# Kernel tuning notes

Measured on AMD Instinct MI355X. Metric: run time of the kernel, lower is better.

Reference implementation:

```python
import jax, jax.numpy as jnp
import numpy as np

GRID_RES = 128
K_PATHS = 8
SIGMA = 0.8
OFFSETS = jnp.array([[0,0,0],[0,0,1],[0,1,0],[0,1,1],[1,0,0],[1,0,1],[1,1,0],[1,1,1]], dtype=jnp.int32)


def setup_inputs() -> dict:
    key = jax.random.key(0)
    ks = jax.random.split(key, 8)
    N = 500000
    M = 500000
    x_source_ref = jax.random.uniform(ks[0], (N, 3), jnp.float32)
    x_source_curr = jnp.clip(x_source_ref + 0.02 * jax.random.normal(ks[1], (N, 3), jnp.float32), 0.0, 1.0)
    x_query_ref = jax.random.uniform(ks[2], (M, 3), jnp.float32)
    def dense(k, fan_in, fan_out):
        return (jax.random.normal(k, (fan_in, fan_out), jnp.float32) / np.sqrt(fan_in)).astype(jnp.float32)
    return {
        'x_query_ref': x_query_ref,
        'x_source_ref': x_source_ref,
        'x_source_curr': x_source_curr,
        'W_f': dense(ks[3], 3, 3), 'b_f': jnp.zeros((3,), jnp.float32),
        'W_d1': dense(ks[4], 24, 64), 'b_d1': jnp.zeros((64,), jnp.float32),
        'W_d2': dense(ks[5], 64, 64), 'b_d2': jnp.zeros((64,), jnp.float32),
        'W_d3': dense(ks[6], 64, 3), 'b_d3': jnp.zeros((3,), jnp.float32),
    }


def _p2g(content, coords):
    # 8-corner trilinear scatter-add: content [N,C] at float coords [N,3] -> flat grid [R^3, C]
    R = GRID_RES
    base = jnp.floor(coords).astype(jnp.int32)            # [N,3]
    d = coords - base.astype(coords.dtype)                # [N,3] fractional part
    off = OFFSETS[:, None, :]                             # [8,1,3]
    w = jnp.prod(jnp.where(off == 1, d[None], 1.0 - d[None]), axis=-1)  # [8,N]
    idx = base[None] + off                                # [8,N,3]
    flat = (idx[..., 0] * R + idx[..., 1]) * R + idx[..., 2]            # [8,N]
    C = content.shape[-1]
    vals = content[None] * w[..., None]                   # [8,N,C]
    return jnp.zeros((R ** 3, C), content.dtype).at[flat.reshape(-1)].add(vals.reshape(-1, C))


def _trilerp(flat_grid, pts):
    # order-1 map_coordinates, mode='nearest': weights from unclipped coords, indices clipped
    R = GRID_RES
    lo = jnp.floor(pts).astype(jnp.int32)                 # [P,3]
    fr = pts - lo.astype(pts.dtype)
    i0 = jnp.clip(lo, 0, R - 1)
    i1 = jnp.clip(lo + 1, 0, R - 1)
    out = jnp.zeros((pts.shape[0], flat_grid.shape[-1]), flat_grid.dtype)
    for c in range(8):  # fixed 8 corners, keeps peak memory at one [P,C] gather at a time
        ox, oy, oz = OFFSETS[c, 0], OFFSETS[c, 1], OFFSETS[c, 2]
        ix = jnp.where(ox == 1, i1[:, 0], i0[:, 0])
        iy = jnp.where(oy == 1, i1[:, 1], i0[:, 1])
        iz = jnp.where(oz == 1, i1[:, 2], i0[:, 2])
        wx = jnp.where(ox == 1, fr[:, 0], 1.0 - fr[:, 0])
        wy = jnp.where(oy == 1, fr[:, 1], 1.0 - fr[:, 1])
        wz = jnp.where(oz == 1, fr[:, 2], 1.0 - fr[:, 2])
        flat = (ix * R + iy) * R + iz
        out = out + flat_grid[flat] * (wx * wy * wz)[:, None]
    return out


def _posenc(x, L=3):
    outs = []
    for i in range(L):
        freq = (2.0 ** i) * jnp.pi
        outs.append(jnp.sin(freq * x))
        outs.append(jnp.cos(freq * x))
    return jnp.concatenate(outs, axis=-1)


def _forward(x_query_ref, x_source_ref, x_source_curr, W_f, b_f, W_d1, b_d1, W_d2, b_d2, W_d3, b_d3):
    R = GRID_RES
    xs = jnp.clip(x_source_ref, 0.0, 1.0)
    xq = jnp.clip(x_query_ref, 0.0, 1.0)
    u = x_source_curr - xs
    f_trans = jax.nn.gelu(u @ W_f + b_f)
    content = jnp.concatenate([f_trans, jnp.ones((u.shape[0], 1), u.dtype), u], axis=-1)  # [N,7]
    coords = jnp.clip(xs * (R - 1), 0.0, R - 1.001)
    flat_grid = _p2g(content, coords)                     # [R^3, 7]
    q = xq * (R - 1)                                      # [M,3]
    M = q.shape[0]
    noise = jax.random.normal(jax.random.key(42), (K_PATHS, M, 3), q.dtype) * SIGMA
    pts = (q[None] + noise).reshape(-1, 3)                # [K*M,3]
    samples = _trilerp(flat_grid, pts).reshape(K_PATHS, M, -1)
    raw = jnp.mean(samples, axis=0)                       # [M,7]
    grid_f, grid_d, grid_u = raw[:, :3], raw[:, 3:4], raw[:, 4:7]
    denom = jnp.maximum(grid_d, 1e-5)
    mask = (grid_d > 1e-5).astype(raw.dtype)
    f_norm = grid_f / denom * mask
    u_norm = grid_u / denom * mask
    dec = jnp.concatenate([f_norm, u_norm, _posenc(xq)], axis=-1)  # [M,24]
    h = jax.nn.gelu(dec @ W_d1 + b_d1)
    h = jax.nn.gelu(h @ W_d2 + b_d2)
    res = h @ W_d3 + b_d3
    return jnp.clip(u_norm + res, 0.001, 0.999)


def reference(x_query_ref, x_source_ref, x_source_curr, W_f, b_f, W_d1, b_d1, W_d2, b_d2, W_d3, b_d3):
    return _forward(x_query_ref, x_source_ref, x_source_curr, W_f, b_f, W_d1, b_d1, W_d2, b_d2, W_d3, b_d3)
```

## Files before the change

### kernel.cpp

```cpp
#include <hip/hip_runtime.h>
#include <cstdint>

#ifndef JAX_PARTITIONABLE
#define JAX_PARTITIONABLE 1
#endif

#define NCELLS (128*128*128)
#define SCAN_BLOCKS 1024
#define NQBINS (32*32*32)

typedef _Float16 f16;
typedef f16  half8 __attribute__((ext_vector_type(8)));
typedef f16  half4 __attribute__((ext_vector_type(4)));
typedef float f32x4 __attribute__((ext_vector_type(4)));

#define WSTR 40
#define DSTR 40
#define W2STR 72

#define GRID_SCALE 1024.0f
#define GRID_ISCALE 0.0009765625f

__device__ __forceinline__ uint32_t rotl32(uint32_t v, int s){ return (v << s) | (v >> (32 - s)); }

__device__ __forceinline__ void tf2x32(uint32_t& x0, uint32_t& x1){
  const uint32_t k0 = 0u, k1 = 42u;
  const uint32_t k2 = 0x1BD11BDAu ^ k0 ^ k1;
  x0 += k0; x1 += k1;
#define TFR(r) { x0 += x1; x1 = rotl32(x1,(r)); x1 ^= x0; }
  TFR(13) TFR(15) TFR(26) TFR(6)
  x0 += k1; x1 += k2 + 1u;
  TFR(17) TFR(29) TFR(16) TFR(24)
  x0 += k2; x1 += k0 + 2u;
  TFR(13) TFR(15) TFR(26) TFR(6)
  x0 += k0; x1 += k1 + 3u;
  TFR(17) TFR(29) TFR(16) TFR(24)
  x0 += k1; x1 += k2 + 4u;
  TFR(13) TFR(15) TFR(26) TFR(6)
  x0 += k2; x1 += k0 + 5u;
#undef TFR
}

__device__ __forceinline__ float erfinv_xla(float x){
  float w = -log1pf(-x*x);
  float p;
  if (w < 5.0f){
    w -= 2.5f;
    p =  2.81022636e-08f;
    p = fmaf(p,w, 3.43273939e-07f);
    p = fmaf(p,w,-3.5233877e-06f);
    p = fmaf(p,w,-4.39150654e-06f);
    p = fmaf(p,w, 0.00021858087f);
    p = fmaf(p,w,-0.00125372503f);
    p = fmaf(p,w,-0.00417768164f);
    p = fmaf(p,w, 0.246640727f);
    p = fmaf(p,w, 1.50140941f);
  } else {
    w = sqrtf(w) - 3.0f;
    p = -0.000200214257f;
    p = fmaf(p,w, 0.000100950558f);
    p = fmaf(p,w, 0.00134934322f);
    p = fmaf(p,w,-0.00367342844f);
    p = fmaf(p,w, 0.00573950773f);
    p = fmaf(p,w,-0.0076224613f);
    p = fmaf(p,w, 0.00943887047f);
    p = fmaf(p,w, 1.00167406f);
    p = fmaf(p,w, 2.83297682f);
  }
  return p*x;
}

__device__ __forceinline__ float noise_at(uint32_t idx, uint32_t half){
#if JAX_PARTITIONABLE
  (void)half;
  uint32_t x0 = 0u, x1 = idx;
  tf2x32(x0, x1);
  uint32_t bits = x0 ^ x1;
#else
  uint32_t j  = (idx < half) ? idx : (idx - half);
  uint32_t x0 = j, x1 = j + half;
  tf2x32(x0, x1);
  uint32_t bits = (idx < half) ? x0 : x1;
#endif
  float f = __uint_as_float((bits >> 9) | 0x3f800000u) - 1.0f;
  float u = fmaxf(-0.99999994f, fmaf(f, 2.0f, -0.99999994f));
  return (1.41421356f * erfinv_xla(u)) * 0.8f;
}

__device__ __forceinline__ float gelu_f(float x){
  float t = x*x;
  float inner = x * fmaf(0.035677408136f, t, 0.7978845608028654f);
  float e = __expf(2.0f * inner);
  float r = __builtin_amdgcn_rcpf(e + 1.0f);
  return x - x*r;
}

__device__ __forceinline__ uint32_t pack2h_scaled(float a, float b){
  union { f16 h[2]; uint32_t u; } c;
  c.h[0] = (f16)(a * GRID_SCALE);
  c.h[1] = (f16)(b * GRID_SCALE);
  return c.u;
}
__device__ __forceinline__ uint32_t pack2h_raw(float a, float b){
  union { f16 h[2]; uint32_t u; } c;
  c.h[0] = (f16)a;
  c.h[1] = (f16)b;
  return c.u;
}

__device__ __forceinline__ void particle_cell(const float* xsr, int i,
                                              float& sx, float& sy, float& sz,
                                              int& bx, int& by, int& bz,
                                              float& dx, float& dy, float& dz){
  sx = fminf(fmaxf(xsr[3*i+0], 0.0f), 1.0f);
  sy = fminf(fmaxf(xsr[3*i+1], 0.0f), 1.0f);
  sz = fminf(fmaxf(xsr[3*i+2], 0.0f), 1.0f);
  float cx = fminf(fmaxf(sx*127.0f, 0.0f), 126.999f);
  float cy = fminf(fmaxf(sy*127.0f, 0.0f), 126.999f);
  float cz = fminf(fmaxf(sz*127.0f, 0.0f), 126.999f);
  float bxf = floorf(cx), byf = floorf(cy), bzf = floorf(cz);
  bx = (int)bxf; by = (int)byf; bz = (int)bzf;
  dx = cx - bxf; dy = cy - byf; dz = cz - bzf;
}

__device__ __forceinline__ int qbin_of(float qx01, float qy01, float qz01){
  int bx = min((int)(qx01*127.0f), 127) >> 2;
  int by = min((int)(qy01*127.0f), 127) >> 2;
  int bz = min((int)(qz01*127.0f), 127) >> 2;
  return (((bx<<5)+by)<<5)+bz;
}

__global__ void __launch_bounds__(256) hist2_kernel(
    const float* __restrict__ xsr, const float* __restrict__ xq,
    int* __restrict__ cells, int* __restrict__ qcnt,
    uint32_t* __restrict__ pcode, uint32_t* __restrict__ qcode, int N, int M){
  int i = blockIdx.x*256 + threadIdx.x;
  if (i < N){
    float sx,sy,sz,dx,dy,dz; int bx,by,bz;
    particle_cell(xsr,i,sx,sy,sz,bx,by,bz,dx,dy,dz);
    int bin = (((bx<<7)+by)<<7)+bz;
    uint32_t rank = (uint32_t)atomicAdd(&cells[bin], 1);
    pcode[i] = ((uint32_t)bin << 11) | rank;
  }
  if (i < M){
    float qx01 = fminf(fmaxf(xq[3*i+0], 0.0f), 1.0f);
    float qy01 = fminf(fmaxf(xq[3*i+1], 0.0f), 1.0f);
    float qz01 = fminf(fmaxf(xq[3*i+2], 0.0f), 1.0f);
    int qb = qbin_of(qx01,qy01,qz01);
    uint32_t rank = (uint32_t)atomicAdd(&qcnt[qb], 1);
    qcode[i] = ((uint32_t)qb << 17) | rank;
  }
}

__global__ void __launch_bounds__(256) scan1_kernel(int* __restrict__ cells,
                                                    int* __restrict__ bsum){
  __shared__ int lds[256];
  int t = threadIdx.x;
  int base = blockIdx.x*2048 + t*8;
  const int4* c4 = reinterpret_cast<const int4*>(cells + base);
  int4 a0 = c4[0], a1 = c4[1];
  int s = a0.x+a0.y+a0.z+a0.w + a1.x+a1.y+a1.z+a1.w;
  lds[t] = s; __syncthreads();
  for (int off = 1; off < 256; off <<= 1){
    int v = (t >= off) ? lds[t-off] : 0;
    __syncthreads();
    lds[t] += v;
    __syncthreads();
  }
  int run = lds[t] - s;
  if (t == 255) bsum[blockIdx.x] = lds[255];
  int* o = cells + base;
  o[0]=run; run+=a0.x; o[1]=run; run+=a0.y; o[2]=run; run+=a0.z; o[3]=run; run+=a0.w;
  o[4]=run; run+=a1.x; o[5]=run; run+=a1.y; o[6]=run; run+=a1.z; o[7]=run;
}

__global__ void __launch_bounds__(1024) scan2q_kernel(int* __restrict__ bsum,
                                                      const int* __restrict__ qcnt,
                                                      int* __restrict__ qstart){
  __shared__ int lds[1024];
  int t = threadIdx.x;
  int v = bsum[t];
  lds[t] = v; __syncthreads();
  for (int off = 1; off < 1024; off <<= 1){
    int u = (t >= off) ? lds[t-off] : 0;
    __syncthreads();
    lds[t] += u;
    __syncthreads();
  }
  bsum[t] = lds[t] - v;
  __syncthreads();
  int base = t*32;
  int loc[32];
  int s = 0;
#pragma unroll
  for (int j = 0; j < 32; ++j){ loc[j] = qcnt[base+j]; s += loc[j]; }
  lds[t] = s; __syncthreads();
  for (int off = 1; off < 1024; off <<= 1){
    int u = (t >= off) ? lds[t-off] : 0;
    __syncthreads();
    lds[t] += u;
    __syncthreads();
  }
  int run = lds[t] - s;
#pragma unroll
  for (int j = 0; j < 32; ++j){ qstart[base+j] = run; run += loc[j]; }
}

__global__ void __launch_bounds__(256) scatter2_kernel(
    const float* __restrict__ xsr, const float* __restrict__ xsc,
    const float* __restrict__ Wf,  const float* __restrict__ bf,
    const float* __restrict__ xq,
    const int* __restrict__ cells, const int* __restrict__ bsum,
    const int* __restrict__ qstart,
    const uint32_t* __restrict__ pcode, const uint32_t* __restrict__ qcode,
    half8* __restrict__ pp, float* __restrict__ pz,
    float4* __restrict__ qpk, int N, int M){
  int i = blockIdx.x*256 + threadIdx.x;
  if (i < N){
    float sx,sy,sz,dx,dy,dz; int bx,by,bz;
    particle_cell(xsr,i,sx,sy,sz,bx,by,bz,dx,dy,dz);
    float ux = xsc[3*i+0] - sx;
    float uy = xsc[3*i+1] - sy;
    float uz = xsc[3*i+2] - sz;
    float f0 = gelu_f(ux*Wf[0] + uy*Wf[3] + uz*Wf[6] + bf[0]);
    float f1 = gelu_f(ux*Wf[1] + uy*Wf[4] + uz*Wf[7] + bf[1]);
    float f2 = gelu_f(ux*Wf[2] + uy*Wf[5] + uz*Wf[8] + bf[2]);
    uint32_t pc = pcode[i];
    int bin  = (int)(pc >> 11);
    int rank = (int)(pc & 2047u);
    int pos = cells[bin] + bsum[bin >> 11] + rank;
    half8 ph;
    ph[0] = (f16)(f0*GRID_SCALE); ph[1] = (f16)(f1*GRID_SCALE); ph[2] = (f16)(f2*GRID_SCALE);
    ph[3] = (f16)(ux*GRID_SCALE); ph[4] = (f16)(uy*GRID_SCALE); ph[5] = (f16)(uz*GRID_SCALE);
    ph[6] = (f16)dx; ph[7] = (f16)dy;
    pp[pos] = ph;
    pz[pos] = dz;
  }
  if (i < M){
    float qx01 = fminf(fmaxf(xq[3*i+0], 0.0f), 1.0f);
    float qy01 = fminf(fmaxf(xq[3*i+1], 0.0f), 1.0f);
    float qz01 = fminf(fmaxf(xq[3*i+2], 0.0f), 1.0f);
    uint32_t qc = qcode[i];
    int qb   = (int)(qc >> 17);
    int rank = (int)(qc & 131071u);
    int pos = qstart[qb] + rank;
    qpk[pos] = make_float4(qx01, qy01, qz01, __int_as_float(i));
  }
}

__global__ void __launch_bounds__(256) p2g_gather_pair_kernel(
    const int* __restrict__ cells, const int* __restrict__ bsum,
    const half8* __restrict__ pp, const float* __restrict__ pz,
    uint4* __restrict__ gridh, int N){
  int tid = blockIdx.x*256 + threadIdx.x;
  int zg = tid & 63, y = (tid >> 6) & 127, x = tid >> 13;
  int z0 = zg << 1;
  auto S = [&](int b){ return cells[b] + bsum[b >> 11]; };
  float a0[2]={0,0},a1[2]={0,0},a2[2]={0,0},a3[2]={0,0},a4[2]={0,0},a5[2]={0,0},a6[2]={0,0};
#pragma unroll
  for (int ox = 0; ox < 2; ++ox){
    int bx = x - ox; if (bx < 0) continue;
#pragma unroll
    for (int oy = 0; oy < 2; ++oy){
      int by = y - oy; if (by < 0) continue;
      int b0 = ((((bx<<7)+by)<<7)) + z0;
      int em = S(b0);
      int sm = (z0 > 0) ? S(b0-1) : em;
      int e0 = S(b0+1);
      int e1 = (b0+2 < NCELLS) ? S(b0+2) : N;
      for (int p = sm; p < e1; ++p){
        half8 P = pp[p]; float dz = pz[p];
        float pdx = (float)P[6], pdy = (float)P[7];
        float wx = ox ? pdx : 1.0f - pdx;
        float wy = oy ? pdy : 1.0f - pdy;
        float wxy = wx*wy;
        float omdz = 1.0f - dz;
        float w0 = (p < em) ? dz : ((p < e0) ? omdz : 0.0f);
        float w1 = (p < em) ? 0.0f : ((p < e0) ? dz : omdz);
        w0 *= wxy; w1 *= wxy;
        float v0=(float)P[0], v1=(float)P[1], v2=(float)P[2];
        float v3=(float)P[3], v4=(float)P[4], v5=(float)P[5];
        a0[0]=fmaf(v0,w0,a0[0]); a1[0]=fmaf(v1,w0,a1[0]); a2[0]=fmaf(v2,w0,a2[0]);
        a3[0]+=w0; a4[0]=fmaf(v3,w0,a4[0]); a5[0]=fmaf(v4,w0,a5[0]); a6[0]=fmaf(v5,w0,a6[0]);
        a0[1]=fmaf(v0,w1,a0[1]); a1[1]=fmaf(v1,w1,a1[1]); a2[1]=fmaf(v2,w1,a2[1]);
        a3[1]+=w1; a4[1]=fmaf(v3,w1,a4[1]); a5[1]=fmaf(v4,w1,a5[1]); a6[1]=fmaf(v5,w1,a6[1]);
      }
    }
  }
  int cell0 = ((((x<<7)+y)<<7)) + z0;
  uint4 g0, g1;
  g0.x = pack2h_raw(a0[0], a1[0]); g0.y = pack2h_raw(a2[0], a4[0]);
  g0.z = pack2h_raw(a5[0], a6[0]); g0.w = __float_as_uint(a3[0]);
  g1.x = pack2h_raw(a0[1], a1[1]); g1.y = pack2h_raw(a2[1], a4[1]);
  g1.z = pack2h_raw(a5[1], a6[1]); g1.w = __float_as_uint(a3[1]);
  uint4* g = gridh + cell0;
  g[0] = g0; g[1] = g1;
}

__global__ void __launch_bounds__(256, 4) gather_mlp_sorted_kernel(
    const float4* __restrict__ qpk,
    const uint4* __restrict__ gridh,
    const float* __restrict__ W1,  const float* __restrict__ b1,
    const float* __restrict__ W2,  const float* __restrict__ b2,
    const float* __restrict__ W3,  const float* __restrict__ b3,
    float* __restrict__ out, int M, int nblk)
{
  __shared__ __align__(16) f16  decs[4][64*DSTR];
  __shared__ __align__(16) f16  w1t[64*WSTR];
  __shared__ __align__(16) f16  w2t[64*W2STR];
  __shared__ __align__(16) float b1s[64], b2s[64];
  __shared__ __align__(16) float w3s[64*4];

  for (int i = threadIdx.x; i < 64*32; i += 256){
    int n = i >> 5, k = i & 31;
    w1t[n*WSTR + k] = (k < 24) ? (f16)W1[k*64 + n] : (f16)0.0f;
  }
  for (int i = threadIdx.x; i < 64*64; i += 256){
    int n = i >> 6, k = i & 63;
    w2t[n*W2STR + k] = (f16)W2[k*64 + n];
  }
  if (threadIdx.x < 64){ b1s[threadIdx.x] = b1[threadIdx.x]; b2s[threadIdx.x] = b2[threadIdx.x]; }
  for (int i = threadIdx.x; i < 192; i += 256){
    w3s[(i/3)*4 + (i - (i/3)*3)] = W3[i];
  }
  __syncthreads();

  int b = blockIdx.x;
  int nb8 = (nblk >> 3) << 3;
  int c = (b < nb8) ? ((b & 7)*(nblk >> 3) + (b >> 3)) : b;
  int t = c*256 + (int)threadIdx.x;
  bool active = (t < M);
  int tc = active ? t : (M - 1);

  float4 qv = qpk[tc];
  float qx01 = qv.x, qy01 = qv.y, qz01 = qv.z;
  int m = __float_as_int(qv.w);
  float qx = qx01*127.0f, qy = qy01*127.0f, qz = qz01*127.0f;

  const uint32_t KSTRIDE = 3u*(uint32_t)M;
  const uint32_t HALF    = 4u*KSTRIDE;
  uint32_t m3 = 3u*(uint32_t)m;
  float nx[8], ny[8], nz[8];
#pragma unroll
  for (int k = 0; k < 8; ++k) {
    uint32_t base = (uint32_t)k*KSTRIDE + m3;
    nx[k] = noise_at(base+0u, HALF);
    ny[k] = noise_at(base+1u, HALF);
    nz[k] = noise_at(base+2u, HALF);
  }

  float r0=0.f,r1=0.f,r2=0.f,r3=0.f,r4=0.f,r5=0.f,r6=0.f;
#pragma unroll
  for (int k = 0; k < 8; ++k) {
    float px = qx + nx[k];
    float py = qy + ny[k];
    float pz = qz + nz[k];
    float fxf = floorf(px), fyf = floorf(py), fzf = floorf(pz);
    float fx = px - fxf, fy = py - fyf, fz = pz - fzf;
    int lx = (int)fxf, ly = (int)fyf, lz = (int)fzf;
    int x0i = min(max(lx,0),127),   x1i = min(max(lx+1,0),127);
    int y0i = min(max(ly,0),127),   y1i = min(max(ly+1,0),127);
    int z0i = min(max(lz,0),127),   z1i = min(max(lz+1,0),127);
    float ex = 1.0f-fx, ey = 1.0f-fy, ez = 1.0f-fz;

    auto corner = [&](int xi,int yi,int zi,float w){
      uint4 q4 = gridh[(((xi<<7)+yi)<<7)+zi];
      union { uint32_t u; f16 h[2]; } c0, c1, c2;
      c0.u = q4.x; c1.u = q4.y; c2.u = q4.z;
      r0 = fmaf((float)c0.h[0], w, r0);
      r1 = fmaf((float)c0.h[1], w, r1);
      r2 = fmaf((float)c1.h[0], w, r2);
      r4 = fmaf((float)c1.h[1], w, r4);
      r5 = fmaf((float)c2.h[0], w, r5);
      r6 = fmaf((float)c2.h[1], w, r6);
      r3 = fmaf(__uint_as_float(q4.w), w, r3);
    };
    corner(x0i,y0i,z0i, ex*ey*ez);
    corner(x0i,y0i,z1i, ex*ey*fz);
    corner(x0i,y1i,z0i, ex*fy*ez);
    corner(x0i,y1i,z1i, ex*fy*fz);
    corner(x1i,y0i,z0i, fx*ey*ez);
    corner(x1i,y0i,z1i, fx*ey*fz);
    corner(x1i,y1i,z0i, fx*fy*ez);
    corner(x1i,y1i,z1i, fx*fy*fz);
  }

  float dmean = r3*0.125f;
  float denom = fmaxf(dmean, 1e-5f);
  float maskf = (dmean > 1e-5f) ? 1.0f : 0.0f;
  float s   = 0.125f/denom*maskf;
  float sfu = s * GRID_ISCALE;
  float un0 = r4*sfu, un1 = r5*sfu, un2 = r6*sfu;

  float dec[24];
  dec[0]=r0*sfu; dec[1]=r1*sfu; dec[2]=r2*sfu; dec[3]=un0; dec[4]=un1; dec[5]=un2;
  dec[6]  = __builtin_amdgcn_sinf(0.5f*qx01);
  dec[7]  = __builtin_amdgcn_sinf(0.5f*qy01);
  dec[8]  = __builtin_amdgcn_sinf(0.5f*qz01);
  dec[9]  = __builtin_amdgcn_cosf(0.5f*qx01);
  dec[10] = __builtin_amdgcn_cosf(0.5f*qy01);
  dec[11] = __builtin_amdgcn_cosf(0.5f*qz01);
  dec[12] = __builtin_amdgcn_sinf(qx01);
  dec[13] = __builtin_amdgcn_sinf(qy01);
  dec[14] = __builtin_amdgcn_sinf(qz01);
  dec[15] = __builtin_amdgcn_cosf(qx01);
  dec[16] = __builtin_amdgcn_cosf(qy01);
  dec[17] = __builtin_amdgcn_cosf(qz01);
  dec[18] = __builtin_amdgcn_sinf(2.0f*qx01);
  dec[19] = __builtin_amdgcn_sinf(2.0f*qy01);
  dec[20] = __builtin_amdgcn_sinf(2.0f*qz01);
  dec[21] = __builtin_amdgcn_cosf(2.0f*qx01);
  dec[22] = __builtin_amdgcn_cosf(2.0f*qy01);
  dec[23] = __builtin_amdgcn_cosf(2.0f*qz01);

  int lane = threadIdx.x & 63;
  int wv   = threadIdx.x >> 6;
  f16* hb = &decs[wv][0];
  int lo = lane & 15;
  int hi = lane >> 4;

  {
    half8 dh;
#pragma unroll
    for (int c4 = 0; c4 < 3; ++c4){
#pragma unroll
      for (int j = 0; j < 8; ++j) dh[j] = (f16)dec[c4*8 + j];
      *reinterpret_cast<half8*>(&hb[lane*DSTR + c4*8]) = dh;
    }
#pragma unroll
    for (int j = 0; j < 8; ++j) dh[j] = (f16)0.0f;
    *reinterpret_cast<half8*>(&hb[lane*DSTR + 24]) = dh;
  }

  half4 w1f[4][2];
#pragma unroll
  for (int a = 0; a < 4; ++a)
#pragma unroll
    for (int kb = 0; kb < 2; ++kb)
      w1f[a][kb] = *reinterpret_cast<const half4*>(&w1t[(16*a + lo)*WSTR + 16*kb + 4*hi]);

  half4 dff[4][2];
#pragma unroll
  for (int bq = 0; bq < 4; ++bq)
#pragma unroll
    for (int kb = 0; kb < 2; ++kb)
      dff[bq][kb] = *reinterpret_cast<const half4*>(&hb[(16*bq + lo)*DSTR + 16*kb + 4*hi]);

  half4 hv[4][4];
#pragma unroll
  for (int a = 0; a < 4; ++a){
    f32x4 zb = *reinterpret_cast<const f32x4*>(&b1s[16*a + 4*hi]);
#pragma unroll
    for (int bq = 0; bq < 4; ++bq){
      f32x4 z = __builtin_amdgcn_mfma_f32_16x16x16f16(w1f[a][0], dff[bq][0], zb, 0, 0, 0);
      z       = __builtin_amdgcn_mfma_f32_16x16x16f16(w1f[a][1], dff[bq][1], z,  0, 0, 0);
      half4 hvv;
#pragma unroll
      for (int p = 0; p < 4; ++p) hvv[p] = (f16)gelu_f(z[p]);
      hv[a][bq] = hvv;
    }
  }

  float part[4][3];
#pragma unroll
  for (int bq = 0; bq < 4; ++bq){ part[bq][0]=0.f; part[bq][1]=0.f; part[bq][2]=0.f; }

#pragma unroll
  for (int a2 = 0; a2 < 4; ++a2){
    half4 w2f[4];
#pragma unroll
    for (int kb = 0; kb < 4; ++kb)
      w2f[kb] = *reinterpret_cast<const half4*>(&w2t[(16*a2 + lo)*W2STR + 16*kb + 4*hi]);
    f32x4 zb2 = *reinterpret_cast<const f32x4*>(&b2s[16*a2 + 4*hi]);
#pragma unroll
    for (int bq = 0; bq < 4; ++bq){
      f32x4 z = __builtin_amdgcn_mfma_f32_16x16x16f16(w2f[0], hv[0][bq], zb2, 0, 0, 0);
      z       = __builtin_amdgcn_mfma_f32_16x16x16f16(w2f[1], hv[1][bq], z,   0, 0, 0);
      z       = __builtin_amdgcn_mfma_f32_16x16x16f16(w2f[2], hv[2][bq], z,   0, 0, 0);
      z       = __builtin_amdgcn_mfma_f32_16x16x16f16(w2f[3], hv[3][bq], z,   0, 0, 0);
#pragma unroll
      for (int p = 0; p < 4; ++p){
        f32x4 w3v = *reinterpret_cast<const f32x4*>(&w3s[(16*a2 + 4*hi + p)*4]);
        float g = gelu_f(z[p]);
        part[bq][0] = fmaf(g, w3v[0], part[bq][0]);
        part[bq][1] = fmaf(g, w3v[1], part[bq][1]);
        part[bq][2] = fmaf(g, w3v[2], part[bq][2]);
      }
    }
  }

#pragma unroll
  for (int bq = 0; bq < 4; ++bq)
#pragma unroll
    for (int cc = 0; cc < 3; ++cc){
      float v = part[bq][cc];
      v += __shfl_xor(v, 16, 64);
      v += __shfl_xor(v, 32, 64);
      part[bq][cc] = v;
    }

  float o0 = (hi==0) ? part[0][0] : (hi==1) ? part[1][0] : (hi==2) ? part[2][0] : part[3][0];
  float o1 = (hi==0) ? part[0][1] : (hi==1) ? part[1][1] : (hi==2) ? part[2][1] : part[3][1];
  float o2 = (hi==0) ? part[0][2] : (hi==1) ? part[1][2] : (hi==2) ? part[2][2] : part[3][2];
  o0 += b3[0]; o1 += b3[1]; o2 += b3[2];

  if (active){
    out[3*m+0] = fminf(fmaxf(un0 + o0, 0.001f), 0.999f);
    out[3*m+1] = fminf(fmaxf(un1 + o1, 0.001f), 0.999f);
    out[3*m+2] = fminf(fmaxf(un2 + o2, 0.001f), 0.999f);
  }
}

__global__ void __launch_bounds__(256) p2g_atomic_kernel(
    const float* __restrict__ xsr, const float* __restrict__ xsc,
    const float* __restrict__ Wf,  const float* __restrict__ bf,
    float* __restrict__ grid, int N)
{
  int i = blockIdx.x*256 + threadIdx.x;
  if (i >= N) return;
  float sx,sy,sz,dx,dy,dz; int bx,by,bz;
  particle_cell(xsr,i,sx,sy,sz,bx,by,bz,dx,dy,dz);
  float ux = xsc[3*i+0] - sx;
  float uy = xsc[3*i+1] - sy;
  float uz = xsc[3*i+2] - sz;
  float f0 = gelu_f(ux*Wf[0] + uy*Wf[3] + uz*Wf[6] + bf[0]);
  float f1 = gelu_f(ux*Wf[1] + uy*Wf[4] + uz*Wf[7] + bf[1]);
  float f2 = gelu_f(ux*Wf[2] + uy*Wf[5] + uz*Wf[8] + bf[2]);
  float ex = 1.0f - dx, ey = 1.0f - dy, ez = 1.0f - dz;
  auto splat = [&](int xi, int yi, int zi, float w){
    float* p = grid + ((size_t)((((xi<<7)+yi)<<7)+zi) << 3);
    unsafeAtomicAdd(p+0, f0*w);
    unsafeAtomicAdd(p+1, f1*w);
    unsafeAtomicAdd(p+2, f2*w);
    unsafeAtomicAdd(p+3, w);
    unsafeAtomicAdd(p+4, ux*w);
    unsafeAtomicAdd(p+5, uy*w);
    unsafeAtomicAdd(p+6, uz*w);
  };
  splat(bx,  by,  bz,   ex*ey*ez);
  splat(bx,  by,  bz+1, ex*ey*dz);
  splat(bx,  by+1,bz,   ex*dy*ez);
  splat(bx,  by+1,bz+1, ex*dy*dz);
  splat(bx+1,by,  bz,   dx*ey*ez);
  splat(bx+1,by,  bz+1, dx*ey*dz);
  splat(bx+1,by+1,bz,   dx*dy*ez);
  splat(bx+1,by+1,bz+1, dx*dy*dz);
}

__global__ void __launch_bounds__(256) grid2half_kernel(
    const float* __restrict__ grid, uint4* __restrict__ gridh){
  int i = blockIdx.x*256 + threadIdx.x;
  const float4* p = reinterpret_cast<const float4*>(grid + ((size_t)i << 3));
  float4 A = p[0], B = p[1];
  uint4 g;
  g.x = pack2h_scaled(A.x, A.y);
  g.y = pack2h_scaled(A.z, B.x);
  g.z = pack2h_scaled(B.y, B.z);
  g.w = __float_as_uint(A.w);
  gridh[i] = g;
}

__global__ void __launch_bounds__(256) qident_kernel(
    const float* __restrict__ xq, float4* __restrict__ qpk, int M){
  int i = blockIdx.x*256 + threadIdx.x;
  if (i >= M) return;
  float qx01 = fminf(fmaxf(xq[3*i+0], 0.0f), 1.0f);
  float qy01 = fminf(fmaxf(xq[3*i+1], 0.0f), 1.0f);
  float qz01 = fminf(fmaxf(xq[3*i+2], 0.0f), 1.0f);
  qpk[i] = make_float4(qx01, qy01, qz01, __int_as_float(i));
}

extern "C" void kernel_launch(void* const* d_in, const int* in_sizes, int n_in,
                              void* d_out, int out_size, void* d_ws, size_t ws_size,
                              hipStream_t stream)
{
  const float* xq  = (const float*)d_in[0];
  const float* xsr = (const float*)d_in[1];
  const float* xsc = (const float*)d_in[2];
  const float* Wf  = (const float*)d_in[3];
  const float* bf  = (const float*)d_in[4];
  const float* W1  = (const float*)d_in[5];
  const float* b1  = (const float*)d_in[6];
  const float* W2  = (const float*)d_in[7];
  const float* b2  = (const float*)d_in[8];
  const float* W3  = (const float*)d_in[9];
  const float* b3  = (const float*)d_in[10];
  float* out  = (float*)d_out;
  int M = in_sizes[0]/3;
  int N = in_sizes[1]/3;

  char* W = (char*)d_ws;
  size_t off = 0;
  auto alloc = [&](size_t bytes){ size_t o = off; off = (off + bytes + 255) & ~(size_t)255; return o; };
  size_t o_gridh = alloc((size_t)NCELLS * 16);
  size_t o_qpk   = alloc((size_t)M * sizeof(float4));
  size_t o_union = off;
  size_t o_cells = alloc((size_t)NCELLS * sizeof(int));
  size_t o_qcnt  = alloc((size_t)NQBINS * sizeof(int));
  size_t o_bsum  = alloc((size_t)SCAN_BLOCKS * sizeof(int));
  size_t o_qstart= alloc((size_t)NQBINS * sizeof(int));
  size_t o_pcode = alloc((size_t)N * sizeof(uint32_t));
  size_t o_qcode = alloc((size_t)M * sizeof(uint32_t));
  size_t o_pp    = alloc((size_t)N * sizeof(half8));
  size_t o_pz    = alloc((size_t)N * sizeof(float));
  size_t main_end = off;
  size_t full_end = (o_union + (size_t)NCELLS * 8 * sizeof(float) > main_end)
                  ? (o_union + (size_t)NCELLS * 8 * sizeof(float)) : main_end;

  uint4*    gridh  = (uint4*)(W + o_gridh);
  float4*   qpk    = (float4*)(W + o_qpk);
  int*      cells  = (int*)(W + o_cells);
  int*      qcnt   = (int*)(W + o_qcnt);
  int*      bsum   = (int*)(W + o_bsum);
  int*      qstart = (int*)(W + o_qstart);
  uint32_t* pcode  = (uint32_t*)(W + o_pcode);
  uint32_t* qcode  = (uint32_t*)(W + o_qcode);
  half8*    pp     = (half8*)(W + o_pp);
  float*    pz     = (float*)(W + o_pz);
  float*    gridf  = (float*)(W + o_union);

  int nthr = (N > M) ? N : M;
  int nblkNM = (nthr + 255) / 256;

  if (main_end <= ws_size) {
    hipMemsetAsync(cells, 0, (size_t)NCELLS * sizeof(int) + (size_t)NQBINS * sizeof(int), stream);
    hist2_kernel<<<nblkNM, 256, 0, stream>>>(xsr, xq, cells, qcnt, pcode, qcode, N, M);
    scan1_kernel<<<SCAN_BLOCKS, 256, 0, stream>>>(cells, bsum);
    scan2q_kernel<<<1, 1024, 0, stream>>>(bsum, qcnt, qstart);
    scatter2_kernel<<<nblkNM, 256, 0, stream>>>(xsr, xsc, Wf, bf, xq, cells, bsum, qstart,
                                                pcode, qcode, pp, pz, qpk, N, M);
    p2g_gather_pair_kernel<<<(NCELLS/2)/256, 256, 0, stream>>>(cells, bsum, pp, pz, gridh, N);
  } else {
    (void)full_end;
    hipMemsetAsync(gridf, 0, (size_t)NCELLS * 8 * sizeof(float), stream);
    p2g_atomic_kernel<<<(N+255)/256, 256, 0, stream>>>(xsr, xsc, Wf, bf, gridf, N);
    grid2half_kernel<<<NCELLS/256, 256, 0, stream>>>(gridf, gridh);
    qident_kernel<<<(M+255)/256, 256, 0, stream>>>(xq, qpk, M);
  }

  int nblk = (M + 255) / 256;
  gather_mlp_sorted_kernel<<<nblk, 256, 0, stream>>>(qpk, gridh, W1,b1,W2,b2,W3,b3, out, M, nblk);
}
```

Baseline: 311.4 us.

## Pack cell counts into 16-bit halves and compute particle payload in histogram pass

```diff
diff --git a/kernel.cpp b/kernel.cpp
--- a/kernel.cpp
+++ b/kernel.cpp
@@ -131,16 +131,33 @@
 }
 
 __global__ void __launch_bounds__(256) hist2_kernel(
-    const float* __restrict__ xsr, const float* __restrict__ xq,
-    int* __restrict__ cells, int* __restrict__ qcnt,
-    uint32_t* __restrict__ pcode, uint32_t* __restrict__ qcode, int N, int M){
+    const float* __restrict__ xsr, const float* __restrict__ xsc,
+    const float* __restrict__ Wf,  const float* __restrict__ bf,
+    const float* __restrict__ xq,
+    int* __restrict__ cells32, int* __restrict__ qcnt,
+    uint32_t* __restrict__ pcode, uint32_t* __restrict__ qcode,
+    half8* __restrict__ pp_u, float* __restrict__ pz_u, int N, int M){
   int i = blockIdx.x*256 + threadIdx.x;
   if (i < N){
     float sx,sy,sz,dx,dy,dz; int bx,by,bz;
     particle_cell(xsr,i,sx,sy,sz,bx,by,bz,dx,dy,dz);
+    float ux = xsc[3*i+0] - sx;
+    float uy = xsc[3*i+1] - sy;
+    float uz = xsc[3*i+2] - sz;
+    float f0 = gelu_f(ux*Wf[0] + uy*Wf[3] + uz*Wf[6] + bf[0]);
+    float f1 = gelu_f(ux*Wf[1] + uy*Wf[4] + uz*Wf[7] + bf[1]);
+    float f2 = gelu_f(ux*Wf[2] + uy*Wf[5] + uz*Wf[8] + bf[2]);
     int bin = (((bx<<7)+by)<<7)+bz;
-    uint32_t rank = (uint32_t)atomicAdd(&cells[bin], 1);
+    int sh = (bin & 1) << 4;
+    uint32_t old = (uint32_t)atomicAdd(&cells32[bin >> 1], 1 << sh);
+    uint32_t rank = (old >> sh) & 2047u;
     pcode[i] = ((uint32_t)bin << 11) | rank;
+    half8 ph;
+    ph[0] = (f16)(f0*GRID_SCALE); ph[1] = (f16)(f1*GRID_SCALE); ph[2] = (f16)(f2*GRID_SCALE);
+    ph[3] = (f16)(ux*GRID_SCALE); ph[4] = (f16)(uy*GRID_SCALE); ph[5] = (f16)(uz*GRID_SCALE);
+    ph[6] = (f16)dx; ph[7] = (f16)dy;
+    pp_u[i] = ph;
+    pz_u[i] = dz;
   }
   if (i < M){
     float qx01 = fminf(fmaxf(xq[3*i+0], 0.0f), 1.0f);
@@ -152,14 +169,17 @@
   }
 }
 
-__global__ void __launch_bounds__(256) scan1_kernel(int* __restrict__ cells,
+__global__ void __launch_bounds__(256) scan1_kernel(int* __restrict__ cells32,
                                                     int* __restrict__ bsum){
   __shared__ int lds[256];
   int t = threadIdx.x;
-  int base = blockIdx.x*2048 + t*8;
-  const int4* c4 = reinterpret_cast<const int4*>(cells + base);
-  int4 a0 = c4[0], a1 = c4[1];
-  int s = a0.x+a0.y+a0.z+a0.w + a1.x+a1.y+a1.z+a1.w;
+  int base = blockIdx.x*1024 + t*4;
+  int4 a = *reinterpret_cast<const int4*>(cells32 + base);
+  int c0 =  a.x        & 0xFFFF, c1 = ((uint32_t)a.x) >> 16;
+  int c2 =  a.y        & 0xFFFF, c3 = ((uint32_t)a.y) >> 16;
+  int c4 =  a.z        & 0xFFFF, c5 = ((uint32_t)a.z) >> 16;
+  int c6 =  a.w        & 0xFFFF, c7 = ((uint32_t)a.w) >> 16;
+  int s = c0+c1+c2+c3+c4+c5+c6+c7;
   lds[t] = s; __syncthreads();
   for (int off = 1; off < 256; off <<= 1){
     int v = (t >= off) ? lds[t-off] : 0;
@@ -167,11 +187,14 @@
     lds[t] += v;
     __syncthreads();
   }
-  int run = lds[t] - s;
+  int e = lds[t] - s;
   if (t == 255) bsum[blockIdx.x] = lds[255];
-  int* o = cells + base;
-  o[0]=run; run+=a0.x; o[1]=run; run+=a0.y; o[2]=run; run+=a0.z; o[3]=run; run+=a0.w;
-  o[4]=run; run+=a1.x; o[5]=run; run+=a1.y; o[6]=run; run+=a1.z; o[7]=run;
+  int4 o;
+  o.x = e | ((e + c0) << 16); e += c0 + c1;
+  o.y = e | ((e + c2) << 16); e += c2 + c3;
+  o.z = e | ((e + c4) << 16); e += c4 + c5;
+  o.w = e | ((e + c6) << 16);
+  *reinterpret_cast<int4*>(cells32 + base) = o;
 }
 
 __global__ void __launch_bounds__(1024) scan2q_kernel(int* __restrict__ bsum,
@@ -207,34 +230,22 @@
 }
 
 __global__ void __launch_bounds__(256) scatter2_kernel(
-    const float* __restrict__ xsr, const float* __restrict__ xsc,
-    const float* __restrict__ Wf,  const float* __restrict__ bf,
     const float* __restrict__ xq,
-    const int* __restrict__ cells, const int* __restrict__ bsum,
+    const int* __restrict__ cells32, const int* __restrict__ bsum,
     const int* __restrict__ qstart,
     const uint32_t* __restrict__ pcode, const uint32_t* __restrict__ qcode,
+    const half8* __restrict__ pp_u, const float* __restrict__ pz_u,
     half8* __restrict__ pp, float* __restrict__ pz,
     float4* __restrict__ qpk, int N, int M){
   int i = blockIdx.x*256 + threadIdx.x;
   if (i < N){
-    float sx,sy,sz,dx,dy,dz; int bx,by,bz;
-    particle_cell(xsr,i,sx,sy,sz,bx,by,bz,dx,dy,dz);
-    float ux = xsc[3*i+0] - sx;
-    float uy = xsc[3*i+1] - sy;
-    float uz = xsc[3*i+2] - sz;
-    float f0 = gelu_f(ux*Wf[0] + uy*Wf[3] + uz*Wf[6] + bf[0]);
-    float f1 = gelu_f(ux*Wf[1] + uy*Wf[4] + uz*Wf[7] + bf[1]);
-    float f2 = gelu_f(ux*Wf[2] + uy*Wf[5] + uz*Wf[8] + bf[2]);
+    const uint16_t* cells16 = reinterpret_cast<const uint16_t*>(cells32);
     uint32_t pc = pcode[i];
     int bin  = (int)(pc >> 11);
     int rank = (int)(pc & 2047u);
-    int pos = cells[bin] + bsum[bin >> 11] + rank;
-    half8 ph;
-    ph[0] = (f16)(f0*GRID_SCALE); ph[1] = (f16)(f1*GRID_SCALE); ph[2] = (f16)(f2*GRID_SCALE);
-    ph[3] = (f16)(ux*GRID_SCALE); ph[4] = (f16)(uy*GRID_SCALE); ph[5] = (f16)(uz*GRID_SCALE);
-    ph[6] = (f16)dx; ph[7] = (f16)dy;
-    pp[pos] = ph;
-    pz[pos] = dz;
+    int pos = (int)cells16[bin] + bsum[bin >> 11] + rank;
+    pp[pos] = pp_u[i];
+    pz[pos] = pz_u[i];
   }
   if (i < M){
     float qx01 = fminf(fmaxf(xq[3*i+0], 0.0f), 1.0f);
@@ -249,13 +260,14 @@
 }
 
 __global__ void __launch_bounds__(256) p2g_gather_pair_kernel(
-    const int* __restrict__ cells, const int* __restrict__ bsum,
+    const int* __restrict__ cells32, const int* __restrict__ bsum,
     const half8* __restrict__ pp, const float* __restrict__ pz,
     uint4* __restrict__ gridh, int N){
   int tid = blockIdx.x*256 + threadIdx.x;
   int zg = tid & 63, y = (tid >> 6) & 127, x = tid >> 13;
   int z0 = zg << 1;
-  auto S = [&](int b){ return cells[b] + bsum[b >> 11]; };
+  const uint16_t* cells16 = reinterpret_cast<const uint16_t*>(cells32);
+  auto S = [&](int b){ return (int)cells16[b] + bsum[b >> 11]; };
   float a0[2]={0,0},a1[2]={0,0},a2[2]={0,0},a3[2]={0,0},a4[2]={0,0},a5[2]={0,0},a6[2]={0,0};
 #pragma unroll
   for (int ox = 0; ox < 2; ++ox){
@@ -595,12 +607,14 @@
   size_t o_gridh = alloc((size_t)NCELLS * 16);
   size_t o_qpk   = alloc((size_t)M * sizeof(float4));
   size_t o_union = off;
-  size_t o_cells = alloc((size_t)NCELLS * sizeof(int));
+  size_t o_cells = alloc((size_t)(NCELLS/2) * sizeof(int));
   size_t o_qcnt  = alloc((size_t)NQBINS * sizeof(int));
   size_t o_bsum  = alloc((size_t)SCAN_BLOCKS * sizeof(int));
   size_t o_qstart= alloc((size_t)NQBINS * sizeof(int));
   size_t o_pcode = alloc((size_t)N * sizeof(uint32_t));
   size_t o_qcode = alloc((size_t)M * sizeof(uint32_t));
+  size_t o_ppu   = alloc((size_t)N * sizeof(half8));
+  size_t o_pzu   = alloc((size_t)N * sizeof(float));
   size_t o_pp    = alloc((size_t)N * sizeof(half8));
   size_t o_pz    = alloc((size_t)N * sizeof(float));
   size_t main_end = off;
@@ -615,6 +629,8 @@
   int*      qstart = (int*)(W + o_qstart);
   uint32_t* pcode  = (uint32_t*)(W + o_pcode);
   uint32_t* qcode  = (uint32_t*)(W + o_qcode);
+  half8*    pp_u   = (half8*)(W + o_ppu);
+  float*    pz_u   = (float*)(W + o_pzu);
   half8*    pp     = (half8*)(W + o_pp);
   float*    pz     = (float*)(W + o_pz);
   float*    gridf  = (float*)(W + o_union);
@@ -622,20 +638,26 @@
   int nthr = (N > M) ? N : M;
   int nblkNM = (nthr + 255) / 256;
 
-  if (main_end <= ws_size) {
-    hipMemsetAsync(cells, 0, (size_t)NCELLS * sizeof(int) + (size_t)NQBINS * sizeof(int), stream);
-    hist2_kernel<<<nblkNM, 256, 0, stream>>>(xsr, xq, cells, qcnt, pcode, qcode, N, M);
+  if (main_end <= ws_size && full_end <= ws_size) {
+    hipMemsetAsync(cells, 0, (size_t)(NCELLS/2) * sizeof(int) + (size_t)NQBINS * sizeof(int), stream);
+    hist2_kernel<<<nblkNM, 256, 0, stream>>>(xsr, xsc, Wf, bf, xq, cells, qcnt,
+                                             pcode, qcode, pp_u, pz_u, N, M);
     scan1_kernel<<<SCAN_BLOCKS, 256, 0, stream>>>(cells, bsum);
     scan2q_kernel<<<1, 1024, 0, stream>>>(bsum, qcnt, qstart);
-    scatter2_kernel<<<nblkNM, 256, 0, stream>>>(xsr, xsc, Wf, bf, xq, cells, bsum, qstart,
-                                                pcode, qcode, pp, pz, qpk, N, M);
+    scatter2_kernel<<<nblkNM, 256, 0, stream>>>(xq, cells, bsum, qstart,
+                                                pcode, qcode, pp_u, pz_u,
+                                                pp, pz, qpk, N, M);
     p2g_gather_pair_kernel<<<(NCELLS/2)/256, 256, 0, stream>>>(cells, bsum, pp, pz, gridh, N);
-  } else {
-    (void)full_end;
+  } else if (full_end <= ws_size) {
     hipMemsetAsync(gridf, 0, (size_t)NCELLS * 8 * sizeof(float), stream);
     p2g_atomic_kernel<<<(N+255)/256, 256, 0, stream>>>(xsr, xsc, Wf, bf, gridf, N);
     grid2half_kernel<<<NCELLS/256, 256, 0, stream>>>(gridf, gridh);
     qident_kernel<<<(M+255)/256, 256, 0, stream>>>(xq, qpk, M);
+  } else {
+    hipMemsetAsync(gridf, 0, (size_t)NCELLS * 8 * sizeof(float), stream);
+    p2g_atomic_kernel<<<(N+255)/256, 256, 0, stream>>>(xsr, xsc, Wf, bf, gridf, N);
+    grid2half_kernel<<<NCELLS/256, 256, 0, stream>>>(gridf, gridh);
+    qident_kernel<<<(M+255)/256, 256, 0, stream>>>(xq, qpk, M);
   }
 
   int nblk = (M + 255) / 256;
```

Result: no change. 311.0 us (-0.1%).
